# Kernel tuning notes

Hardware: AMD Instinct MI355X
Metric: run time of the kernel (lower is better)

The kernel has to match this reference:

```python
import jax, jax.numpy as jnp
import numpy as np

RADII = (0.8, 1.6)
NSAMPLES = (16, 32)
IN_C = 64
BN_EPS = 1e-3  # BN1d eps; eval-mode BN with running stats (0, 1)
B, N_PER, M_PER = 2, 8192, 2048
BOX = (40.0, 40.0, 4.0)  # point cloud extent in meters


def _batch_ids(cnt, total):
    # point i belongs to batch searchsorted(cumsum(cnt), i, 'right')
    return jnp.searchsorted(jnp.cumsum(cnt), jnp.arange(total), side='right')


def _ball_group(xyz, bid, new_xyz, nbid, feats, radius, nsample):
    # Ball query (stacked-batch): first `nsample` points within `radius` of each
    # query, same batch only; pad short balls with the first found index;
    # fully-empty balls are zeroed (pcdet QueryAndGroup semantics).
    d2 = jnp.sum((new_xyz[:, None, :] - xyz[None, :, :]) ** 2, axis=-1)  # (M, N)
    within = (d2 < radius * radius) & (nbid[:, None] == bid[None, :])
    n = xyz.shape[0]
    score = jnp.where(within, -jnp.arange(n, dtype=jnp.float32), -jnp.inf)
    vals, idx = jax.lax.top_k(score, nsample)  # smallest in-ball indices first
    valid = jnp.isfinite(vals)
    idx = jnp.where(valid, idx, idx[:, :1])  # pad with first found index
    empty = ~valid[:, :1]  # (M, 1): no point in ball
    g_xyz = xyz[idx] - new_xyz[:, None, :]          # (M, ns, 3) relative coords
    g = jnp.concatenate([g_xyz, feats[idx]], -1)    # (M, ns, 3 + C), xyz first
    return jnp.where(empty[:, :, None], 0.0, g)


def _shared_mlp(x, layers):
    # Conv1d(k=1, bias=False) + BN1d(eval, mean=0, var=1) + ReLU per layer
    inv_std = 1.0 / jnp.sqrt(1.0 + BN_EPS)
    for w, g, b in layers:
        x = jnp.einsum('mnc,oc->mno', x, w)
        x = jax.nn.relu(x * (g * inv_std) + b)
    return x  # (M, ns, cout)


def setup_inputs() -> dict:
    key = jax.random.key(0)
    ks = jax.random.split(key, 16)
    box = jnp.asarray(BOX, dtype=jnp.float32)
    xyz = jax.random.uniform(ks[0], (B * N_PER, 3), dtype=jnp.float32) * box
    new_xyz = jax.random.uniform(ks[1], (B * M_PER, 3), dtype=jnp.float32) * box
    features = jax.random.normal(ks[2], (B * N_PER, IN_C), dtype=jnp.float32)

    def conv_w(k, cin, cout):
        return jax.random.normal(k, (cout, cin), dtype=jnp.float32) / np.sqrt(cin)

    cin = IN_C + 3  # use_xyz -> +3
    inp = dict(xyz=xyz, features=features, new_xyz=new_xyz,
               w00=conv_w(ks[3], cin, 64), g00=jnp.ones(64), b00=jnp.zeros(64),
               w01=conv_w(ks[4], 64, 64), g01=jnp.ones(64), b01=jnp.zeros(64),
               w10=conv_w(ks[5], cin, 64), g10=jnp.ones(64), b10=jnp.zeros(64),
               w11=conv_w(ks[6], 64, 64), g11=jnp.ones(64), b11=jnp.zeros(64),
               xyz_batch_cnt=jnp.full((B,), N_PER, dtype=jnp.int32),
               new_xyz_batch_cnt=jnp.full((B,), M_PER, dtype=jnp.int32))
    return inp


def reference(xyz, features, new_xyz,
              w00, g00, b00, w01, g01, b01,
              w10, g10, b10, w11, g11, b11,
              xyz_batch_cnt, new_xyz_batch_cnt):
    bid = _batch_ids(xyz_batch_cnt, xyz.shape[0])
    nbid = _batch_ids(new_xyz_batch_cnt, new_xyz.shape[0])
    layer_params = [[(w00, g00, b00), (w01, g01, b01)],
                    [(w10, g10, b10), (w11, g11, b11)]]
    outs = []
    for k in range(len(RADII)):
        g = _ball_group(xyz, bid, new_xyz, nbid, features, RADII[k], NSAMPLES[k])
        h = _shared_mlp(g, layer_params[k])
        outs.append(jnp.max(h, axis=1))  # max-pool over neighbors
    return jnp.concatenate(outs, axis=1)  # (M_tot, 128)
```

## Files before the change

### kernel.cpp

```cpp
#include <hip/hip_runtime.h>
#include <hip/hip_bf16.h>
#include <stdint.h>


#define NS0 16
#define NS1 32
#define NXC 25
#define NYC 25
#define NZC 3
#define CPB (NXC * NYC * NZC)
#define CINV 0.625f
#define CSZ 1.6f
#define CAP 48

typedef _Float16 half8 __attribute__((ext_vector_type(8)));
typedef float f32x4 __attribute__((ext_vector_type(4)));

static __device__ __forceinline__ half8 cvt8(float4 a, float4 b) {
    half8 r;
    r[0] = (_Float16)a.x; r[1] = (_Float16)a.y; r[2] = (_Float16)a.z; r[3] = (_Float16)a.w;
    r[4] = (_Float16)b.x; r[5] = (_Float16)b.y; r[6] = (_Float16)b.z; r[7] = (_Float16)b.w;
    return r;
}
static __device__ __forceinline__ uint32_t pk2(float x, float y) {
    const _Float16 a = (_Float16)x, c = (_Float16)y;
    return (uint32_t)__builtin_bit_cast(uint16_t, a) |
           ((uint32_t)__builtin_bit_cast(uint16_t, c) << 16);
}

__global__ __launch_bounds__(256) void prep(
    const float* __restrict__ w00, const float* __restrict__ g00, const float* __restrict__ b00,
    const float* __restrict__ w01, const float* __restrict__ g01, const float* __restrict__ b01,
    const float* __restrict__ w10, const float* __restrict__ g10, const float* __restrict__ b10,
    const float* __restrict__ w11, const float* __restrict__ g11, const float* __restrict__ b11,
    float* __restrict__ wpk, int* __restrict__ cell_cnt, int n4)
{
    if (blockIdx.x >= 2) {
        const int i = (blockIdx.x - 2) * 256 + threadIdx.x;
        if (i < n4) ((int4*)cell_cnt)[i] = make_int4(0, 0, 0, 0);
        return;
    }
    const int k = blockIdx.x;
    const int tid = threadIdx.x;
    const int lane = tid & 63, t = tid >> 6;
    const int p = lane & 15, h = lane >> 4;
    const float* W1 = k ? w10 : w00; const float* G1 = k ? g10 : g00; const float* B1 = k ? b10 : b00;
    const float* W2 = k ? w11 : w01; const float* G2 = k ? g11 : g01; const float* B2 = k ? b11 : b01;
    const float inv = 1.0f / sqrtf(1.0f + 1e-3f);

    uint32_t* outw = (uint32_t*)wpk + (size_t)k * 6144;
    const int m = 16 * t + p;
    const float sc1 = G1[m] * inv;
    #pragma unroll
    for (int s = 0; s < 3; ++s) {
        #pragma unroll
        for (int r = 0; r < 4; ++r) {
            uint32_t u = 0;
            #pragma unroll
            for (int e = 0; e < 2; ++e) {
                const int cpad = 32 * s + 8 * h + 2 * r + e;
                float val = 0.f;
                if (cpad < 64)       val = W1[m * 67 + 3 + cpad] * sc1;
                else if (cpad < 67)  val = W1[m * 67 + (cpad - 64)] * sc1;
                else if (cpad == 67) val = B1[m];
                const _Float16 hv = (_Float16)val;
                u |= ((uint32_t)__builtin_bit_cast(uint16_t, hv)) << (16 * e);
            }
            outw[((t * 3 + s) * 64 + lane) * 4 + r] = u;
        }
    }
    const float sc2 = G2[m] * inv;
    uint32_t* outw2 = outw + 3072;
    #pragma unroll
    for (int s = 0; s < 2; ++s) {
        #pragma unroll
        for (int r = 0; r < 4; ++r) {
            uint32_t u = 0;
            #pragma unroll
            for (int e = 0; e < 2; ++e) {
                const int cch = 32 * s + 8 * h + 2 * r + e;
                const _Float16 hv = (_Float16)(W2[m * 64 + cch] * sc2);
                u |= ((uint32_t)__builtin_bit_cast(uint16_t, hv)) << (16 * e);
            }
            outw2[((t * 2 + s) * 64 + lane) * 4 + r] = u;
        }
    }
    float* bo = wpk + (size_t)k * 6144 + 5120;
    #pragma unroll
    for (int r = 0; r < 4; ++r)
        bo[(t * 64 + lane) * 4 + r] = B2[16 * t + 4 * h + r];
}

__global__ __launch_bounds__(256) void bin_cap(
    const float* __restrict__ xyz, const int* __restrict__ xcnt, int B, int N,
    int* __restrict__ cell_cnt, float4* __restrict__ binned4)
{
    const int i = blockIdx.x * 256 + threadIdx.x;
    if (i >= N) return;
    int acc = 0, b = 0;
    for (int k = 0; k < B; ++k) { int c = xcnt[k]; if (i >= acc && i < acc + c) b = k; acc += c; }
    const float x = xyz[3 * i], y = xyz[3 * i + 1], z = xyz[3 * i + 2];
    const int cx = min(NXC - 1, max(0, (int)floorf(x * CINV)));
    const int cy = min(NYC - 1, max(0, (int)floorf(y * CINV)));
    const int cz = min(NZC - 1, max(0, (int)floorf(z * CINV)));
    const int cell = b * CPB + (cz * NYC + cy) * NXC + cx;
    const int slot = atomicAdd(&cell_cnt[cell], 1);
    if (slot < CAP) {
        float4 r; r.x = x; r.y = y; r.z = z; r.w = __int_as_float(i);
        binned4[(size_t)cell * CAP + slot] = r;
    }
}

__global__ __launch_bounds__(256) void query_mlp(
    const float* __restrict__ xyz, const float* __restrict__ feats,
    const float* __restrict__ new_xyz, const int* __restrict__ ncnt,
    const int* __restrict__ cell_cnt, const float4* __restrict__ binned4,
    const float* __restrict__ wpk, int B, int M, int TW,
    float* __restrict__ out)
{
    __shared__ uint32_t cand[4][128];
    __shared__ int lidx[4][2][NS0 + NS1];
    __shared__ uint4 hbuf[4][144];

    const int tid = threadIdx.x;
    const int wave = tid >> 6, lane = tid & 63;
    const int gw = blockIdx.x * 4 + wave;
    if (gw >= M) return;
    const int mq0 = gw, mq1 = gw + TW;
    const int nq = (mq1 < M) ? 2 : 1;

    int cnts0[2], cnts1[2];
    float qc0[3], qc1[3];
    uint32_t* cd = cand[wave];
    const unsigned long long lower = (lane == 0) ? 0ull : (~0ull >> (64 - lane));
    const float R0S = 0.64f, R1S = 2.56f;
    const float PAD = 1.60002f;

    #pragma unroll
    for (int qi = 0; qi < 2; ++qi) {
        if (qi < nq) {
            const int m = qi ? mq1 : mq0;
            int acc = 0, b = 0;
            for (int k2 = 0; k2 < B; ++k2) { int c = ncnt[k2]; if (m >= acc && m < acc + c) b = k2; acc += c; }
            const float qx = new_xyz[3 * m], qy = new_xyz[3 * m + 1], qz = new_xyz[3 * m + 2];
            if (qi) { qc1[0] = qx; qc1[1] = qy; qc1[2] = qz; }
            else    { qc0[0] = qx; qc0[1] = qy; qc0[2] = qz; }

            const int lx = max(0, (int)floorf((qx - PAD) * CINV));
            const int hx = min(NXC - 1, (int)floorf((qx + PAD) * CINV));
            const int ly = max(0, (int)floorf((qy - PAD) * CINV));
            const int hy = min(NYC - 1, (int)floorf((qy + PAD) * CINV));
            const int lz = max(0, (int)floorf((qz - PAD) * CINV));
            const int hz = min(NZC - 1, (int)floorf((qz + PAD) * CINV));
            const int wx = hx - lx + 1, wy = hy - ly + 1, wz = hz - lz + 1;
            const int nw = wx * wy * wz;

            int cnt_l = 0, cell_l = 0;
            if (lane < nw) {
                const int wxy = wx * wy;
                const int ldz = lane / wxy;
                const int rem = lane - ldz * wxy;
                const int ldy = rem / wx;
                const int ldx = rem - ldy * wx;
                const int cx = lx + ldx, cy = ly + ldy, cz = lz + ldz;
                const float bx0 = cx * CSZ, by0 = cy * CSZ, bz0 = cz * CSZ;
                const float dx = (qx < bx0) ? (bx0 - qx) : ((qx > bx0 + CSZ) ? (qx - bx0 - CSZ) : 0.f);
                const float dy = (qy < by0) ? (by0 - qy) : ((qy > by0 + CSZ) ? (qy - by0 - CSZ) : 0.f);
                const float dz = (qz < bz0) ? (bz0 - qz) : ((qz > bz0 + CSZ) ? (qz - bz0 - CSZ) : 0.f);
                const float md2 = dx * dx + dy * dy + dz * dz;
                cell_l = b * CPB + (cz * NYC + cy) * NXC + cx;
                if (md2 <= R1S + 1e-3f) cnt_l = min(cell_cnt[cell_l], CAP);
            }

            int incl = cnt_l;
            #pragma unroll
            for (int d = 1; d < 64; d <<= 1) {
                const int v = __shfl_up(incl, d);
                if (lane >= d) incl += v;
            }
            const int excl = incl - cnt_l;
            const int tot = __shfl(incl, 63);

            int c = 0, c0n = 0;
            for (int t0 = 0; t0 < tot; t0 += 64) {
                const int t = t0 + lane;
                const bool v = t < tot;
                int lo = 0, hi = 63;
                #pragma unroll
                for (int s = 0; s < 6; ++s) {
                    const int mid = (lo + hi) >> 1;
                    const int vm = __shfl(incl, mid);
                    if (vm > t) hi = mid; else lo = mid + 1;
                }
                const int j = lo & 63;
                const int slot = t - __shfl(excl, j);
                const int cell = __shfl(cell_l, j);
                float d2 = 1e30f;
                int pid = 0;
                if (v) {
                    const float4 e = binned4[(size_t)cell * CAP + slot];
                    pid = __float_as_int(e.w);
                    const float dx = e.x - qx, dy = e.y - qy, dzp = e.z - qz;
                    d2 = __fadd_rn(__fadd_rn(__fmul_rn(dx, dx), __fmul_rn(dy, dy)),
                                   __fmul_rn(dzp, dzp));
                }
                const bool keep = v && (d2 < R1S);
                const bool f0 = keep && (d2 < R0S);
                const unsigned long long mk = __ballot(keep);
                if (keep) {
                    const int pos = c + __popcll(mk & lower);
                    if (pos < 128) cd[pos] = ((uint32_t)pid << 1) | (f0 ? 1u : 0u);
                }
                c += __popcll(mk);
                c0n += __popcll(__ballot(f0));
            }

            const int cc = min(c, 128);
            int* L = &lidx[wave][qi][0];
            const uint32_t ka = (lane < cc) ? cd[lane] : 0xFFFFFFFFu;
            const uint32_t kb = (64 + lane < cc) ? cd[64 + lane] : 0xFFFFFFFFu;
            int ra = 0, ra0 = 0, rb = 0, rb0 = 0;
            for (int e2 = 0; e2 < cc; e2 += 4) {
                #pragma unroll
                for (int u = 0; u < 4; ++u) {
                    const int ee = e2 + u;
                    if (ee < cc) {
                        const uint32_t ke = cd[ee];
                        const int sm_a = (ke < ka), sm_b = (ke < kb), f = (int)(ke & 1u);
                        ra += sm_a; ra0 += sm_a & f;
                        rb += sm_b; rb0 += sm_b & f;
                    }
                }
            }
            if (lane < cc) {
                const int pid = (int)(ka >> 1);
                if ((ka & 1u) && ra0 < NS0) L[ra0] = pid;
                if (ra < NS1) L[NS0 + ra] = pid;
            }
            if (64 + lane < cc) {
                const int pid = (int)(kb >> 1);
                if ((kb & 1u) && rb0 < NS0) L[rb0] = pid;
                if (rb < NS1) L[NS0 + rb] = pid;
            }
            if (qi) { cnts1[0] = min(c0n, NS0); cnts1[1] = min(c, NS1); }
            else    { cnts0[0] = min(c0n, NS0); cnts0[1] = min(c, NS1); }
        }
    }

    const int p = lane & 15, h = lane >> 4;
    char* hb = (char*)&hbuf[wave][0];

    #pragma unroll
    for (int k = 0; k < 2; ++k) {
        const uint4* wp = (const uint4*)((const uint32_t*)wpk + (size_t)k * 6144);
        half8 a1[4][3], a2[4][2];
        #pragma unroll
        for (int t = 0; t < 4; ++t)
            #pragma unroll
            for (int s = 0; s < 3; ++s)
                a1[t][s] = __builtin_bit_cast(half8, wp[(t * 3 + s) * 64 + lane]);
        const uint4* wp2 = wp + 768;
        #pragma unroll
        for (int t = 0; t < 4; ++t)
            #pragma unroll
            for (int s = 0; s < 2; ++s)
                a2[t][s] = __builtin_bit_cast(half8, wp2[(t * 2 + s) * 64 + lane]);
        const float4* bp2 = (const float4*)((const float*)wpk + (size_t)k * 6144 + 5120);
        const float4 b2r_[4] = { bp2[0 * 64 + lane], bp2[1 * 64 + lane],
                                 bp2[2 * 64 + lane], bp2[3 * 64 + lane] };

        #pragma unroll
        for (int qi = 0; qi < 2; ++qi) {
            if (qi < nq) {
                const int m = qi ? mq1 : mq0;
                const int c_pts = qi ? cnts1[k] : cnts0[k];
                const float qx = qi ? qc1[0] : qc0[0];
                const float qy = qi ? qc1[1] : qc0[1];
                const float qz = qi ? qc1[2] : qc0[2];
                const int ntmax = k ? 2 : 1;
                const int nt = min((c_pts + 15) >> 4, ntmax);
                const int* L = &lidx[wave][qi][0];

                f32x4 rmax[4] = {f32x4(0.f), f32x4(0.f), f32x4(0.f), f32x4(0.f)};

                half8 b0a[2], b1a[2], b2a[2];
                bool ona[2];
                #pragma unroll
                for (int pt = 0; pt < 2; ++pt) {
                    b0a[pt] = 0; b1a[pt] = 0; b2a[pt] = 0; ona[pt] = false;
                    if (pt < nt) {
                        const int gp = pt * 16 + p;
                        const bool on = gp < c_pts;
                        ona[pt] = on;
                        if (on) {
                            const int j = L[k ? (NS0 + gp) : gp];
                            const float4* f0p = (const float4*)(feats + (size_t)j * 64 + 8 * h);
                            const float4* f1p = (const float4*)(feats + (size_t)j * 64 + 32 + 8 * h);
                            b0a[pt] = cvt8(f0p[0], f0p[1]);
                            b1a[pt] = cvt8(f1p[0], f1p[1]);
                            if (h == 0) {
                                half8 b2 = 0;
                                b2[0] = (_Float16)(xyz[3 * j + 0] - qx);
                                b2[1] = (_Float16)(xyz[3 * j + 1] - qy);
                                b2[2] = (_Float16)(xyz[3 * j + 2] - qz);
                                b2[3] = (_Float16)1.0f;
                                b2a[pt] = b2;
                            }
                        }
                    }
                }

                #pragma unroll
                for (int pt = 0; pt < 2; ++pt) {
                    if (pt < nt) {
                        f32x4 acc[4] = {f32x4(0.f), f32x4(0.f), f32x4(0.f), f32x4(0.f)};
                        #pragma unroll
                        for (int t = 0; t < 4; ++t) {
                            acc[t] = __builtin_amdgcn_mfma_f32_16x16x32_f16(a1[t][0], b0a[pt], acc[t], 0, 0, 0);
                            acc[t] = __builtin_amdgcn_mfma_f32_16x16x32_f16(a1[t][1], b1a[pt], acc[t], 0, 0, 0);
                            acc[t] = __builtin_amdgcn_mfma_f32_16x16x32_f16(a1[t][2], b2a[pt], acc[t], 0, 0, 0);
                        }
                        #pragma unroll
                        for (int t = 0; t < 4; ++t) {
                            *(uint32_t*)(hb + 144 * p + 32 * t + 8 * h) =
                                pk2(fmaxf(acc[t][0], 0.f), fmaxf(acc[t][1], 0.f));
                            *(uint32_t*)(hb + 144 * p + 32 * t + 8 * h + 4) =
                                pk2(fmaxf(acc[t][2], 0.f), fmaxf(acc[t][3], 0.f));
                        }
                        const half8 g0 = *(const half8*)(hb + 144 * p + 16 * h);
                        const half8 g1 = *(const half8*)(hb + 144 * p + 64 + 16 * h);

                        f32x4 acc2[4] = {f32x4(0.f), f32x4(0.f), f32x4(0.f), f32x4(0.f)};
                        #pragma unroll
                        for (int t = 0; t < 4; ++t) {
                            acc2[t] = __builtin_amdgcn_mfma_f32_16x16x32_f16(a2[t][0], g0, acc2[t], 0, 0, 0);
                            acc2[t] = __builtin_amdgcn_mfma_f32_16x16x32_f16(a2[t][1], g1, acc2[t], 0, 0, 0);
                        }
                        #pragma unroll
                        for (int t = 0; t < 4; ++t)
                            #pragma unroll
                            for (int r = 0; r < 4; ++r) {
                                const float v = ona[pt] ? (acc2[t][r] + b2r_[t][r]) : 0.f;
                                rmax[t][r] = fmaxf(rmax[t][r], v);
                            }
                    }
                }

                #pragma unroll
                for (int d = 1; d < 16; d <<= 1)
                    #pragma unroll
                    for (int t = 0; t < 4; ++t)
                        #pragma unroll
                        for (int r = 0; r < 4; ++r)
                            rmax[t][r] = fmaxf(rmax[t][r], __shfl_xor(rmax[t][r], d));

                if (p == 0) {
                    float* o = out + (size_t)m * 128 + k * 64 + 4 * h;
                    #pragma unroll
                    for (int t = 0; t < 4; ++t) {
                        float4 v = make_float4(rmax[t][0], rmax[t][1], rmax[t][2], rmax[t][3]);
                        *(float4*)(o + 16 * t) = v;
                    }
                }
            }
        }
    }
}

extern "C" void kernel_launch(void* const* d_in, const int* in_sizes, int n_in,
                              void* d_out, int out_size, void* d_ws, size_t ws_size,
                              hipStream_t stream) {
    const float* xyz     = (const float*)d_in[0];
    const float* feats   = (const float*)d_in[1];
    const float* new_xyz = (const float*)d_in[2];
    const float* w00 = (const float*)d_in[3];
    const float* g00 = (const float*)d_in[4];
    const float* b00 = (const float*)d_in[5];
    const float* w01 = (const float*)d_in[6];
    const float* g01 = (const float*)d_in[7];
    const float* b01 = (const float*)d_in[8];
    const float* w10 = (const float*)d_in[9];
    const float* g10 = (const float*)d_in[10];
    const float* b10 = (const float*)d_in[11];
    const float* w11 = (const float*)d_in[12];
    const float* g11 = (const float*)d_in[13];
    const float* b11 = (const float*)d_in[14];
    const int* xcnt = (const int*)d_in[15];
    const int* ncnt = (const int*)d_in[16];

    const int B = in_sizes[15];
    const int N = in_sizes[0] / 3;
    const int M = in_sizes[2] / 3;
    const int ncells = B * CPB;
    const int ncells_pad = (ncells + 3) & ~3;

    uint32_t* w32 = (uint32_t*)d_ws;
    float* wpk      = (float*)w32;
    int* cell_cnt   = (int*)(w32 + 12288);
    float4* binned4 = (float4*)(cell_cnt + ncells_pad);

    const int n4 = ncells_pad >> 2;
    const int zero_blocks = (n4 + 255) / 256;
    prep<<<2 + zero_blocks, 256, 0, stream>>>(
        w00, g00, b00, w01, g01, b01, w10, g10, b10, w11, g11, b11,
        wpk, cell_cnt, n4);
    bin_cap<<<(N + 255) / 256, 256, 0, stream>>>(xyz, xcnt, B, N,
                                                 cell_cnt, binned4);
    const int blocks = (M + 7) / 8;
    const int TW = blocks * 4;
    query_mlp<<<blocks, 256, 0, stream>>>(xyz, feats, new_xyz, ncnt,
                                          cell_cnt, binned4, wpk, B, M, TW,
                                          (float*)d_out);
}
```

Before: 37.87 us.

## Stage MLP weights in LDS, one query per wave, defer bias+ReLU past max-pool

Each wave now handles one query instead of two, and the grid doubles. Per-lane register-held weight fragments are replaced by staging each scale's packed weights into shared memory with block-wide syncs, which cuts register pressure and may raise occupancy. The layer-2 bias and ReLU are applied once after the neighbour max-pool rather than per point, which is valid because both are monotone. In exchange, LDS traffic and barriers are added, weights are reloaded per block, and per-wave reuse across two queries is lost.

```diff
diff --git a/kernel.cpp b/kernel.cpp
--- a/kernel.cpp
+++ b/kernel.cpp
@@ -111,260 +111,264 @@
     }
 }
 
+static __device__ __forceinline__ void mlp_one(
+    int c_pts, int ntmax, const int* __restrict__ L,
+    float qx, float qy, float qz,
+    const uint4* __restrict__ wlds, char* __restrict__ hb,
+    const float* __restrict__ xyz, const float* __restrict__ feats,
+    const float4* __restrict__ bq, float* __restrict__ out_base,
+    bool qvalid, int lane)
+{
+    const int p = lane & 15, h = lane >> 4;
+    const int nt = min((c_pts + 15) >> 4, ntmax);
+
+    f32x4 macc[4] = {f32x4(-3e38f), f32x4(-3e38f), f32x4(-3e38f), f32x4(-3e38f)};
+
+    half8 b0a[2], b1a[2], b2a[2];
+    bool ona[2];
+    #pragma unroll
+    for (int pt = 0; pt < 2; ++pt) {
+        b0a[pt] = 0; b1a[pt] = 0; b2a[pt] = 0; ona[pt] = false;
+        if (pt < nt) {
+            const int gp = pt * 16 + p;
+            const bool on = gp < c_pts;
+            ona[pt] = on;
+            if (on) {
+                const int j = L[gp];
+                const float4* f0p = (const float4*)(feats + (size_t)j * 64 + 8 * h);
+                const float4* f1p = (const float4*)(feats + (size_t)j * 64 + 32 + 8 * h);
+                b0a[pt] = cvt8(f0p[0], f0p[1]);
+                b1a[pt] = cvt8(f1p[0], f1p[1]);
+                if (h == 0) {
+                    half8 b2 = 0;
+                    b2[0] = (_Float16)(xyz[3 * j + 0] - qx);
+                    b2[1] = (_Float16)(xyz[3 * j + 1] - qy);
+                    b2[2] = (_Float16)(xyz[3 * j + 2] - qz);
+                    b2[3] = (_Float16)1.0f;
+                    b2a[pt] = b2;
+                }
+            }
+        }
+    }
+
+    #pragma unroll
+    for (int pt = 0; pt < 2; ++pt) {
+        if (pt < nt) {
+            f32x4 acc[4] = {f32x4(0.f), f32x4(0.f), f32x4(0.f), f32x4(0.f)};
+            #pragma unroll
+            for (int t = 0; t < 4; ++t) {
+                #pragma unroll
+                for (int s = 0; s < 3; ++s) {
+                    const half8 a = __builtin_bit_cast(half8, wlds[(t * 3 + s) * 64 + lane]);
+                    const half8 bf = (s == 0) ? b0a[pt] : ((s == 1) ? b1a[pt] : b2a[pt]);
+                    acc[t] = __builtin_amdgcn_mfma_f32_16x16x32_f16(a, bf, acc[t], 0, 0, 0);
+                }
+            }
+            #pragma unroll
+            for (int t = 0; t < 4; ++t) {
+                *(uint32_t*)(hb + 144 * p + 32 * t + 8 * h) =
+                    pk2(fmaxf(acc[t][0], 0.f), fmaxf(acc[t][1], 0.f));
+                *(uint32_t*)(hb + 144 * p + 32 * t + 8 * h + 4) =
+                    pk2(fmaxf(acc[t][2], 0.f), fmaxf(acc[t][3], 0.f));
+            }
+            const half8 g0 = *(const half8*)(hb + 144 * p + 16 * h);
+            const half8 g1 = *(const half8*)(hb + 144 * p + 64 + 16 * h);
+
+            f32x4 acc2[4] = {f32x4(0.f), f32x4(0.f), f32x4(0.f), f32x4(0.f)};
+            #pragma unroll
+            for (int t = 0; t < 4; ++t) {
+                #pragma unroll
+                for (int s = 0; s < 2; ++s) {
+                    const half8 a = __builtin_bit_cast(half8, wlds[768 + (t * 2 + s) * 64 + lane]);
+                    const half8 bf = (s == 0) ? g0 : g1;
+                    acc2[t] = __builtin_amdgcn_mfma_f32_16x16x32_f16(a, bf, acc2[t], 0, 0, 0);
+                }
+            }
+            #pragma unroll
+            for (int t = 0; t < 4; ++t)
+                #pragma unroll
+                for (int r = 0; r < 4; ++r)
+                    if (ona[pt]) macc[t][r] = fmaxf(macc[t][r], acc2[t][r]);
+        }
+    }
+
+    #pragma unroll
+    for (int d = 1; d < 16; d <<= 1)
+        #pragma unroll
+        for (int t = 0; t < 4; ++t)
+            #pragma unroll
+            for (int r = 0; r < 4; ++r)
+                macc[t][r] = fmaxf(macc[t][r], __shfl_xor(macc[t][r], d));
+
+    if (p == 0 && qvalid) {
+        float* o = out_base + 4 * h;
+        #pragma unroll
+        for (int t = 0; t < 4; ++t) {
+            const float4 bb = bq[t * 64 + lane];
+            float4 v;
+            v.x = fmaxf(macc[t][0] + bb.x, 0.f);
+            v.y = fmaxf(macc[t][1] + bb.y, 0.f);
+            v.z = fmaxf(macc[t][2] + bb.z, 0.f);
+            v.w = fmaxf(macc[t][3] + bb.w, 0.f);
+            *(float4*)(o + 16 * t) = v;
+        }
+    }
+}
+
 __global__ __launch_bounds__(256) void query_mlp(
     const float* __restrict__ xyz, const float* __restrict__ feats,
     const float* __restrict__ new_xyz, const int* __restrict__ ncnt,
     const int* __restrict__ cell_cnt, const float4* __restrict__ binned4,
-    const float* __restrict__ wpk, int B, int M, int TW,
+    const float* __restrict__ wpk, int B, int M,
     float* __restrict__ out)
 {
+    __shared__ uint4 wlds[1280];
     __shared__ uint32_t cand[4][128];
-    __shared__ int lidx[4][2][NS0 + NS1];
+    __shared__ int lidx[4][NS0 + NS1];
     __shared__ uint4 hbuf[4][144];
 
     const int tid = threadIdx.x;
     const int wave = tid >> 6, lane = tid & 63;
     const int gw = blockIdx.x * 4 + wave;
-    if (gw >= M) return;
-    const int mq0 = gw, mq1 = gw + TW;
-    const int nq = (mq1 < M) ? 2 : 1;
-
-    int cnts0[2], cnts1[2];
-    float qc0[3], qc1[3];
-    uint32_t* cd = cand[wave];
-    const unsigned long long lower = (lane == 0) ? 0ull : (~0ull >> (64 - lane));
-    const float R0S = 0.64f, R1S = 2.56f;
-    const float PAD = 1.60002f;
-
-    #pragma unroll
-    for (int qi = 0; qi < 2; ++qi) {
-        if (qi < nq) {
-            const int m = qi ? mq1 : mq0;
-            int acc = 0, b = 0;
-            for (int k2 = 0; k2 < B; ++k2) { int c = ncnt[k2]; if (m >= acc && m < acc + c) b = k2; acc += c; }
-            const float qx = new_xyz[3 * m], qy = new_xyz[3 * m + 1], qz = new_xyz[3 * m + 2];
-            if (qi) { qc1[0] = qx; qc1[1] = qy; qc1[2] = qz; }
-            else    { qc0[0] = qx; qc0[1] = qy; qc0[2] = qz; }
-
-            const int lx = max(0, (int)floorf((qx - PAD) * CINV));
-            const int hx = min(NXC - 1, (int)floorf((qx + PAD) * CINV));
-            const int ly = max(0, (int)floorf((qy - PAD) * CINV));
-            const int hy = min(NYC - 1, (int)floorf((qy + PAD) * CINV));
-            const int lz = max(0, (int)floorf((qz - PAD) * CINV));
-            const int hz = min(NZC - 1, (int)floorf((qz + PAD) * CINV));
-            const int wx = hx - lx + 1, wy = hy - ly + 1, wz = hz - lz + 1;
-            const int nw = wx * wy * wz;
-
-            int cnt_l = 0, cell_l = 0;
-            if (lane < nw) {
-                const int wxy = wx * wy;
-                const int ldz = lane / wxy;
-                const int rem = lane - ldz * wxy;
-                const int ldy = rem / wx;
-                const int ldx = rem - ldy * wx;
-                const int cx = lx + ldx, cy = ly + ldy, cz = lz + ldz;
-                const float bx0 = cx * CSZ, by0 = cy * CSZ, bz0 = cz * CSZ;
-                const float dx = (qx < bx0) ? (bx0 - qx) : ((qx > bx0 + CSZ) ? (qx - bx0 - CSZ) : 0.f);
-                const float dy = (qy < by0) ? (by0 - qy) : ((qy > by0 + CSZ) ? (qy - by0 - CSZ) : 0.f);
-                const float dz = (qz < bz0) ? (bz0 - qz) : ((qz > bz0 + CSZ) ? (qz - bz0 - CSZ) : 0.f);
-                const float md2 = dx * dx + dy * dy + dz * dz;
-                cell_l = b * CPB + (cz * NYC + cy) * NXC + cx;
-                if (md2 <= R1S + 1e-3f) cnt_l = min(cell_cnt[cell_l], CAP);
-            }
-
-            int incl = cnt_l;
-            #pragma unroll
-            for (int d = 1; d < 64; d <<= 1) {
-                const int v = __shfl_up(incl, d);
-                if (lane >= d) incl += v;
-            }
-            const int excl = incl - cnt_l;
-            const int tot = __shfl(incl, 63);
-
-            int c = 0, c0n = 0;
-            for (int t0 = 0; t0 < tot; t0 += 64) {
-                const int t = t0 + lane;
-                const bool v = t < tot;
-                int lo = 0, hi = 63;
-                #pragma unroll
-                for (int s = 0; s < 6; ++s) {
-                    const int mid = (lo + hi) >> 1;
-                    const int vm = __shfl(incl, mid);
-                    if (vm > t) hi = mid; else lo = mid + 1;
+    const bool qvalid = gw < M;
+    const int m = qvalid ? gw : 0;
+
+    {
+        const uint4* ws = (const uint4*)((const uint32_t*)wpk);
+        #pragma unroll
+        for (int i = 0; i < 5; ++i) wlds[tid + 256 * i] = ws[tid + 256 * i];
+    }
+
+    int cA = 0, cB = 0;
+    float qx, qy, qz;
+    {
+        int acc = 0, b = 0;
+        for (int k2 = 0; k2 < B; ++k2) { int c = ncnt[k2]; if (m >= acc && m < acc + c) b = k2; acc += c; }
+        qx = new_xyz[3 * m]; qy = new_xyz[3 * m + 1]; qz = new_xyz[3 * m + 2];
+        const float R0S = 0.64f, R1S = 2.56f;
+        const float PAD = 1.60002f;
+
+        const int lx = max(0, (int)floorf((qx - PAD) * CINV));
+        const int hx = min(NXC - 1, (int)floorf((qx + PAD) * CINV));
+        const int ly = max(0, (int)floorf((qy - PAD) * CINV));
+        const int hy = min(NYC - 1, (int)floorf((qy + PAD) * CINV));
+        const int lz = max(0, (int)floorf((qz - PAD) * CINV));
+        const int hz = min(NZC - 1, (int)floorf((qz + PAD) * CINV));
+        const int wx = hx - lx + 1, wy = hy - ly + 1, wz = hz - lz + 1;
+        const int nw = wx * wy * wz;
+
+        int cnt_l = 0, cell_l = 0;
+        if (lane < nw) {
+            const int wxy = wx * wy;
+            const int ldz = lane / wxy;
+            const int rem = lane - ldz * wxy;
+            const int ldy = rem / wx;
+            const int ldx = rem - ldy * wx;
+            const int cx = lx + ldx, cy = ly + ldy, cz = lz + ldz;
+            const float bx0 = cx * CSZ, by0 = cy * CSZ, bz0 = cz * CSZ;
+            const float dx = (qx < bx0) ? (bx0 - qx) : ((qx > bx0 + CSZ) ? (qx - bx0 - CSZ) : 0.f);
+            const float dy = (qy < by0) ? (by0 - qy) : ((qy > by0 + CSZ) ? (qy - by0 - CSZ) : 0.f);
+            const float dz = (qz < bz0) ? (bz0 - qz) : ((qz > bz0 + CSZ) ? (qz - bz0 - CSZ) : 0.f);
+            const float md2 = dx * dx + dy * dy + dz * dz;
+            cell_l = b * CPB + (cz * NYC + cy) * NXC + cx;
+            if (md2 <= R1S + 1e-3f) cnt_l = min(cell_cnt[cell_l], CAP);
+        }
+
+        int incl = cnt_l;
+        #pragma unroll
+        for (int d = 1; d < 64; d <<= 1) {
+            const int v = __shfl_up(incl, d);
+            if (lane >= d) incl += v;
+        }
+        const int excl = incl - cnt_l;
+        const int tot = __shfl(incl, 63);
+
+        uint32_t* cd = cand[wave];
+        const unsigned long long lower = (lane == 0) ? 0ull : (~0ull >> (64 - lane));
+        int c = 0, c0n = 0;
+
+        for (int t0 = 0; t0 < tot; t0 += 64) {
+            const int t = t0 + lane;
+            const bool v = t < tot;
+            int lo = 0, hi = 63;
+            #pragma unroll
+            for (int s = 0; s < 6; ++s) {
+                const int mid = (lo + hi) >> 1;
+                const int vm = __shfl(incl, mid);
+                if (vm > t) hi = mid; else lo = mid + 1;
+            }
+            const int j = lo & 63;
+            const int slot = t - __shfl(excl, j);
+            const int cell = __shfl(cell_l, j);
+            float d2 = 1e30f;
+            int pid = 0;
+            if (v) {
+                const float4 e = binned4[(size_t)cell * CAP + slot];
+                pid = __float_as_int(e.w);
+                const float dx = e.x - qx, dy = e.y - qy, dzp = e.z - qz;
+                d2 = __fadd_rn(__fadd_rn(__fmul_rn(dx, dx), __fmul_rn(dy, dy)),
+                               __fmul_rn(dzp, dzp));
+            }
+            const bool keep = v && (d2 < R1S);
+            const bool f0 = keep && (d2 < R0S);
+            const unsigned long long mk = __ballot(keep);
+            if (keep) {
+                const int pos = c + __popcll(mk & lower);
+                if (pos < 128) cd[pos] = ((uint32_t)pid << 1) | (f0 ? 1u : 0u);
+            }
+            c += __popcll(mk);
+            c0n += __popcll(__ballot(f0));
+        }
+
+        const int cc = min(c, 128);
+        int* L = &lidx[wave][0];
+        const uint32_t ka = (lane < cc) ? cd[lane] : 0xFFFFFFFFu;
+        const uint32_t kb = (64 + lane < cc) ? cd[64 + lane] : 0xFFFFFFFFu;
+        int ra = 0, ra0 = 0, rb = 0, rb0 = 0;
+        for (int e2 = 0; e2 < cc; e2 += 4) {
+            #pragma unroll
+            for (int u = 0; u < 4; ++u) {
+                const int ee = e2 + u;
+                if (ee < cc) {
+                    const uint32_t ke = cd[ee];
+                    const int sm_a = (ke < ka), sm_b = (ke < kb), f = (int)(ke & 1u);
+                    ra += sm_a; ra0 += sm_a & f;
+                    rb += sm_b; rb0 += sm_b & f;
                 }
-                const int j = lo & 63;
-                const int slot = t - __shfl(excl, j);
-                const int cell = __shfl(cell_l, j);
-                float d2 = 1e30f;
-                int pid = 0;
-                if (v) {
-                    const float4 e = binned4[(size_t)cell * CAP + slot];
-                    pid = __float_as_int(e.w);
-                    const float dx = e.x - qx, dy = e.y - qy, dzp = e.z - qz;
-                    d2 = __fadd_rn(__fadd_rn(__fmul_rn(dx, dx), __fmul_rn(dy, dy)),
-                                   __fmul_rn(dzp, dzp));
-                }
-                const bool keep = v && (d2 < R1S);
-                const bool f0 = keep && (d2 < R0S);
-                const unsigned long long mk = __ballot(keep);
-                if (keep) {
-                    const int pos = c + __popcll(mk & lower);
-                    if (pos < 128) cd[pos] = ((uint32_t)pid << 1) | (f0 ? 1u : 0u);
-                }
-                c += __popcll(mk);
-                c0n += __popcll(__ballot(f0));
-            }
-
-            const int cc = min(c, 128);
-            int* L = &lidx[wave][qi][0];
-            const uint32_t ka = (lane < cc) ? cd[lane] : 0xFFFFFFFFu;
-            const uint32_t kb = (64 + lane < cc) ? cd[64 + lane] : 0xFFFFFFFFu;
-            int ra = 0, ra0 = 0, rb = 0, rb0 = 0;
-            for (int e2 = 0; e2 < cc; e2 += 4) {
-                #pragma unroll
-                for (int u = 0; u < 4; ++u) {
-                    const int ee = e2 + u;
-                    if (ee < cc) {
-                        const uint32_t ke = cd[ee];
-                        const int sm_a = (ke < ka), sm_b = (ke < kb), f = (int)(ke & 1u);
-                        ra += sm_a; ra0 += sm_a & f;
-                        rb += sm_b; rb0 += sm_b & f;
-                    }
-                }
-            }
-            if (lane < cc) {
-                const int pid = (int)(ka >> 1);
-                if ((ka & 1u) && ra0 < NS0) L[ra0] = pid;
-                if (ra < NS1) L[NS0 + ra] = pid;
-            }
-            if (64 + lane < cc) {
-                const int pid = (int)(kb >> 1);
-                if ((kb & 1u) && rb0 < NS0) L[rb0] = pid;
-                if (rb < NS1) L[NS0 + rb] = pid;
-            }
-            if (qi) { cnts1[0] = min(c0n, NS0); cnts1[1] = min(c, NS1); }
-            else    { cnts0[0] = min(c0n, NS0); cnts0[1] = min(c, NS1); }
-        }
-    }
-
-    const int p = lane & 15, h = lane >> 4;
+            }
+        }
+        if (lane < cc) {
+            const int pid = (int)(ka >> 1);
+            if ((ka & 1u) && ra0 < NS0) L[ra0] = pid;
+            if (ra < NS1) L[NS0 + ra] = pid;
+        }
+        if (64 + lane < cc) {
+            const int pid = (int)(kb >> 1);
+            if ((kb & 1u) && rb0 < NS0) L[rb0] = pid;
+            if (rb < NS1) L[NS0 + rb] = pid;
+        }
+        cA = min(c0n, NS0);
+        cB = min(c, NS1);
+    }
+
+    __syncthreads();
+
     char* hb = (char*)&hbuf[wave][0];
-
-    #pragma unroll
-    for (int k = 0; k < 2; ++k) {
-        const uint4* wp = (const uint4*)((const uint32_t*)wpk + (size_t)k * 6144);
-        half8 a1[4][3], a2[4][2];
-        #pragma unroll
-        for (int t = 0; t < 4; ++t)
-            #pragma unroll
-            for (int s = 0; s < 3; ++s)
-                a1[t][s] = __builtin_bit_cast(half8, wp[(t * 3 + s) * 64 + lane]);
-        const uint4* wp2 = wp + 768;
-        #pragma unroll
-        for (int t = 0; t < 4; ++t)
-            #pragma unroll
-            for (int s = 0; s < 2; ++s)
-                a2[t][s] = __builtin_bit_cast(half8, wp2[(t * 2 + s) * 64 + lane]);
-        const float4* bp2 = (const float4*)((const float*)wpk + (size_t)k * 6144 + 5120);
-        const float4 b2r_[4] = { bp2[0 * 64 + lane], bp2[1 * 64 + lane],
-                                 bp2[2 * 64 + lane], bp2[3 * 64 + lane] };
-
-        #pragma unroll
-        for (int qi = 0; qi < 2; ++qi) {
-            if (qi < nq) {
-                const int m = qi ? mq1 : mq0;
-                const int c_pts = qi ? cnts1[k] : cnts0[k];
-                const float qx = qi ? qc1[0] : qc0[0];
-                const float qy = qi ? qc1[1] : qc0[1];
-                const float qz = qi ? qc1[2] : qc0[2];
-                const int ntmax = k ? 2 : 1;
-                const int nt = min((c_pts + 15) >> 4, ntmax);
-                const int* L = &lidx[wave][qi][0];
-
-                f32x4 rmax[4] = {f32x4(0.f), f32x4(0.f), f32x4(0.f), f32x4(0.f)};
-
-                half8 b0a[2], b1a[2], b2a[2];
-                bool ona[2];
-                #pragma unroll
-                for (int pt = 0; pt < 2; ++pt) {
-                    b0a[pt] = 0; b1a[pt] = 0; b2a[pt] = 0; ona[pt] = false;
-                    if (pt < nt) {
-                        const int gp = pt * 16 + p;
-                        const bool on = gp < c_pts;
-                        ona[pt] = on;
-                        if (on) {
-                            const int j = L[k ? (NS0 + gp) : gp];
-                            const float4* f0p = (const float4*)(feats + (size_t)j * 64 + 8 * h);
-                            const float4* f1p = (const float4*)(feats + (size_t)j * 64 + 32 + 8 * h);
-                            b0a[pt] = cvt8(f0p[0], f0p[1]);
-                            b1a[pt] = cvt8(f1p[0], f1p[1]);
-                            if (h == 0) {
-                                half8 b2 = 0;
-                                b2[0] = (_Float16)(xyz[3 * j + 0] - qx);
-                                b2[1] = (_Float16)(xyz[3 * j + 1] - qy);
-                                b2[2] = (_Float16)(xyz[3 * j + 2] - qz);
-                                b2[3] = (_Float16)1.0f;
-                                b2a[pt] = b2;
-                            }
-                        }
-                    }
-                }
-
-                #pragma unroll
-                for (int pt = 0; pt < 2; ++pt) {
-                    if (pt < nt) {
-                        f32x4 acc[4] = {f32x4(0.f), f32x4(0.f), f32x4(0.f), f32x4(0.f)};
-                        #pragma unroll
-                        for (int t = 0; t < 4; ++t) {
-                            acc[t] = __builtin_amdgcn_mfma_f32_16x16x32_f16(a1[t][0], b0a[pt], acc[t], 0, 0, 0);
-                            acc[t] = __builtin_amdgcn_mfma_f32_16x16x32_f16(a1[t][1], b1a[pt], acc[t], 0, 0, 0);
-                            acc[t] = __builtin_amdgcn_mfma_f32_16x16x32_f16(a1[t][2], b2a[pt], acc[t], 0, 0, 0);
-                        }
-                        #pragma unroll
-                        for (int t = 0; t < 4; ++t) {
-                            *(uint32_t*)(hb + 144 * p + 32 * t + 8 * h) =
-                                pk2(fmaxf(acc[t][0], 0.f), fmaxf(acc[t][1], 0.f));
-                            *(uint32_t*)(hb + 144 * p + 32 * t + 8 * h + 4) =
-                                pk2(fmaxf(acc[t][2], 0.f), fmaxf(acc[t][3], 0.f));
-                        }
-                        const half8 g0 = *(const half8*)(hb + 144 * p + 16 * h);
-                        const half8 g1 = *(const half8*)(hb + 144 * p + 64 + 16 * h);
-
-                        f32x4 acc2[4] = {f32x4(0.f), f32x4(0.f), f32x4(0.f), f32x4(0.f)};
-                        #pragma unroll
-                        for (int t = 0; t < 4; ++t) {
-                            acc2[t] = __builtin_amdgcn_mfma_f32_16x16x32_f16(a2[t][0], g0, acc2[t], 0, 0, 0);
-                            acc2[t] = __builtin_amdgcn_mfma_f32_16x16x32_f16(a2[t][1], g1, acc2[t], 0, 0, 0);
-                        }
-                        #pragma unroll
-                        for (int t = 0; t < 4; ++t)
-                            #pragma unroll
-                            for (int r = 0; r < 4; ++r) {
-                                const float v = ona[pt] ? (acc2[t][r] + b2r_[t][r]) : 0.f;
-                                rmax[t][r] = fmaxf(rmax[t][r], v);
-                            }
-                    }
-                }
-
-                #pragma unroll
-                for (int d = 1; d < 16; d <<= 1)
-                    #pragma unroll
-                    for (int t = 0; t < 4; ++t)
-                        #pragma unroll
-                        for (int r = 0; r < 4; ++r)
-                            rmax[t][r] = fmaxf(rmax[t][r], __shfl_xor(rmax[t][r], d));
-
-                if (p == 0) {
-                    float* o = out + (size_t)m * 128 + k * 64 + 4 * h;
-                    #pragma unroll
-                    for (int t = 0; t < 4; ++t) {
-                        float4 v = make_float4(rmax[t][0], rmax[t][1], rmax[t][2], rmax[t][3]);
-                        *(float4*)(o + 16 * t) = v;
-                    }
-                }
-            }
-        }
-    }
+    mlp_one(cA, 1, &lidx[wave][0], qx, qy, qz, wlds, hb, xyz, feats,
+            (const float4*)(wpk + 5120), out + (size_t)m * 128, qvalid, lane);
+
+    __syncthreads();
+
+    {
+        const uint4* ws = (const uint4*)((const uint32_t*)wpk + 6144);
+        #pragma unroll
+        for (int i = 0; i < 5; ++i) wlds[tid + 256 * i] = ws[tid + 256 * i];
+    }
+    __syncthreads();
+
+    mlp_one(cB, 2, &lidx[wave][NS0], qx, qy, qz, wlds, hb, xyz, feats,
+            (const float4*)(wpk + 6144 + 5120), out + (size_t)m * 128 + 64,
+            qvalid, lane);
 }
 
 extern "C" void kernel_launch(void* const* d_in, const int* in_sizes, int n_in,
@@ -406,9 +410,7 @@
         wpk, cell_cnt, n4);
     bin_cap<<<(N + 255) / 256, 256, 0, stream>>>(xyz, xcnt, B, N,
                                                  cell_cnt, binned4);
-    const int blocks = (M + 7) / 8;
-    const int TW = blocks * 4;
-    query_mlp<<<blocks, 256, 0, stream>>>(xyz, feats, new_xyz, ncnt,
-                                          cell_cnt, binned4, wpk, B, M, TW,
-                                          (float*)d_out);
-}
+    query_mlp<<<(M + 3) / 4, 256, 0, stream>>>(xyz, feats, new_xyz, ncnt,
+                                               cell_cnt, binned4, wpk, B, M,
+                                               (float*)d_out);
+}
```

Result: faster. 33.53 us (-11.5%).
